# Optimization experiments

Measured on AMD Instinct MI355X. Metric: run time of the kernel, lower is better.

Reference implementation:

```python
import jax, jax.numpy as jnp
import numpy as np

KERNEL = 5
STRIDE = 1
DN = ('NHWC', 'HWIO', 'NHWC')
PRIOR_VAR = 0.01


def setup_inputs() -> dict:
    key = jax.random.key(0)
    k1, k2, k3 = jax.random.split(key, 3)
    mu_in = jax.random.normal(k1, (32, 224, 224, 3), dtype=jnp.float32)
    # GlorotNormal-ish scale for a 5x5x3 -> 64 kernel
    w_mu = jax.random.normal(k2, (5, 5, 3, 64), dtype=jnp.float32) * 0.12
    # original init: uniform in [min_sigma, ini_sigma] = [-4.6, -2.25]
    w_sigma = jax.random.uniform(k3, (64,), dtype=jnp.float32, minval=-4.6, maxval=-2.25)
    return {"mu_in": mu_in, "w_mu": w_mu, "w_sigma": w_sigma}


def reference(mu_in, w_mu, w_sigma):
    # KL regularizer: broadcast of (64,) logvar against (5,5,3,64) mu, mean over all
    kl = 0.5 * jnp.mean(
        jnp.log(PRIOR_VAR) - 1.0 - w_sigma
        + jax.nn.softplus(w_sigma) / PRIOR_VAR
        + jnp.square(w_mu) / PRIOR_VAR
    )

    w_sigma_2 = jax.nn.softplus(w_sigma)  # log(1+exp(w_sigma))

    # Mean path: standard conv2d, VALID, stride 1, NHWC
    mu_out = jax.lax.conv_general_dilated(
        mu_in, w_mu, (STRIDE, STRIDE), 'VALID', dimension_numbers=DN
    )  # [B, Ho, Wo, K]

    # Variance path: per-output-location sum over the k*k*C patch of x^2 / x_dim.
    # Same math as the original extract_patches + reduce_sum, but computed as a
    # channel-summed box filter on x^2 (no im2col materialization).
    C = mu_in.shape[-1]
    x_dim = jnp.asarray(KERNEL * KERNEL * C, mu_in.dtype)
    ones_k = jnp.ones((KERNEL, KERNEL, C, 1), mu_in.dtype)
    sq = jax.lax.conv_general_dilated(
        jnp.square(mu_in), ones_k, (STRIDE, STRIDE), 'VALID', dimension_numbers=DN
    ) / x_dim  # [B, Ho, Wo, 1]

    Sigma_out = jax.nn.softplus(w_sigma_2 * sq)  # broadcast -> [B, Ho, Wo, K]
    return (mu_out, Sigma_out, kl)
```

## Files before the change

### kernel.cpp

```cpp
#include <hip/hip_runtime.h>
#include <math.h>

#define BATCH 32
#define HIN   224
#define WIN   224
#define CIN   3
#define KOUT  64
#define RK    5
#define HOUT  220
#define WOUT  220

#define NTOT ((size_t)BATCH * HOUT * WOUT * KOUT)

typedef float  v4f    __attribute__((ext_vector_type(4)));
typedef short  short8 __attribute__((ext_vector_type(8)));

#define WS_WF_FRAGS 768
#define WS_WSG_OFF  12288

__device__ __forceinline__ float exp2_hw(float x) { float r; asm("v_exp_f32 %0, %1" : "=v"(r) : "v"(x)); return r; }
__device__ __forceinline__ float log2_hw(float x) { float r; asm("v_log_f32 %0, %1" : "=v"(r) : "v"(x)); return r; }
#define LOG2E 1.44269504088896f
#define LN2   0.69314718055995f

__device__ __forceinline__ float softplus_hw(float x) {
    float t = exp2_hw(-fabsf(x) * LOG2E);
    return fmaxf(x, 0.0f) + LN2 * log2_hw(1.0f + t);
}
__device__ __forceinline__ float softplus_pos(float y) {
    return y + LN2 * log2_hw(1.0f + exp2_hw(-y * LOG2E));
}
__device__ __forceinline__ short f2bf(float x) {
    unsigned u = __float_as_uint(x);
    u = (u + 0x7FFFu + ((u >> 16) & 1u)) >> 16;
    return (short)u;
}

__global__ __launch_bounds__(256) void vdp_prep_kernel(
    const float* __restrict__ w_mu, const float* __restrict__ w_sigma,
    void* __restrict__ ws, float* __restrict__ out)
{
    __shared__ float red[4];
    short8* wf = (short8*)ws;
    float* wsg = (float*)((char*)ws + WS_WSG_OFF);
    const int t = threadIdx.x;

    for (int f = t; f < WS_WF_FRAGS; f += 256) {
        const int s  = f >> 8;
        const int nb = (f >> 6) & 3;
        const int l  = f & 63;
        const int ch = nb * 16 + (l & 15);
        const int h2 = l >> 4;
        short8 r;
        #pragma unroll
        for (int i = 0; i < 8; ++i) {
            const int k = s * 32 + h2 * 8 + i;
            const int kh = k >> 4, inner = k & 15;
            float v = 0.0f;
            if (inner < 15 && k < 80) {
                const int kw = inner / 3;
                const int c  = inner - kw * 3;
                v = w_mu[((kh * 5 + kw) * 3 + c) * KOUT + ch];
            }
            r[i] = f2bf(v);
        }
        wf[f] = r;
    }
    if (t < KOUT) wsg[t] = softplus_hw(w_sigma[t]);

    float s = 0.0f;
    for (int i = t; i < RK * RK * CIN * KOUT; i += 256) {
        const float v = w_mu[i];
        s = fmaf(v, v, s);
    }
    float u = s * (100.0f / 4800.0f);
    if (t < KOUT) {
        const float wsv = w_sigma[t];
        u += (-wsv + softplus_hw(wsv) * 100.0f) * (1.0f / 64.0f);
    }
    #pragma unroll
    for (int off = 32; off > 0; off >>= 1)
        u += __shfl_down(u, off, 64);
    if ((t & 63) == 0) red[t >> 6] = u;
    __syncthreads();
    if (t == 0) {
        const float U = red[0] + red[1] + red[2] + red[3];
        out[2 * NTOT] = 0.5f * (-4.6051701860f - 1.0f + U);
    }
}

__global__ __launch_bounds__(256, 4) void vdp_conv_kernel(
    const float* __restrict__ mu_in, const void* __restrict__ ws, float* __restrict__ out)
{
    __shared__ float s_row[8][112];
    __shared__ float s_ssq[8][40];
    __shared__ float s_sq[4][32];

    const int tid  = threadIdx.x;
    const int lane = tid & 63;
    const int wid  = tid >> 6;
    const int p    = lane & 15;
    const int h2   = lane >> 4;

    const int b  = blockIdx.z;
    const int r0 = blockIdx.y * 4;
    const int x0 = blockIdx.x * 32;

    const short8* wfg = (const short8*)ws;
    short8 wf[12];
    #pragma unroll
    for (int f = 0; f < 12; ++f) wf[f] = wfg[f * 64 + lane];
    const float* wsg_g = (const float*)((const char*)ws + WS_WSG_OFF);
    const v4f wsg_kg = *(const v4f*)(wsg_g + p * 4);

    const size_t inbase = ((size_t)b * HIN + r0) * (WIN * CIN);
    for (int idx = tid; idx < 8 * 112; idx += 256) {
        const int r = idx / 112, c = idx - r * 112;
        int f = x0 * 3 + c; if (f > WIN * CIN - 1) f = WIN * CIN - 1;
        s_row[r][c] = mu_in[inbase + (size_t)r * (WIN * CIN) + f];
    }
    __syncthreads();

    for (int idx = tid; idx < 8 * 36; idx += 256) {
        const int r = idx / 36, px = idx - r * 36;
        const float a0 = s_row[r][3 * px], a1 = s_row[r][3 * px + 1], a2 = s_row[r][3 * px + 2];
        s_ssq[r][px] = fmaf(a0, a0, fmaf(a1, a1, a2 * a2));
    }
    __syncthreads();

    if (tid < 128) {
        const int orow = tid >> 5, pc = tid & 31;
        float a = 0.0f;
        #pragma unroll
        for (int kh = 0; kh < RK; ++kh)
            #pragma unroll
            for (int kw = 0; kw < RK; ++kw)
                a += s_ssq[orow + kh][pc + kw];
        s_sq[orow][pc] = a * (1.0f / 75.0f);
    }
    __syncthreads();

    const int rt = wid;
    const size_t rowbase = (((size_t)b * HOUT + r0 + rt) * WOUT + x0) * KOUT;

    #pragma unroll
    for (int g = 0; g < 2; ++g) {
        short8 pf[3];
        #pragma unroll
        for (int s = 0; s < 3; ++s) {
            int ridx = rt + 2 * s + (h2 >> 1);
            ridx = ridx > 7 ? 7 : ridx;
            const float* rp = &s_row[ridx][3 * (16 * g + p) + 8 * (h2 & 1)];
            short8 r;
            #pragma unroll
            for (int i = 0; i < 8; ++i) r[i] = f2bf(rp[i]);
            pf[s] = r;
        }
        v4f acc[4];
        #pragma unroll
        for (int nb = 0; nb < 4; ++nb) {
            v4f a = {0.0f, 0.0f, 0.0f, 0.0f};
            #pragma unroll
            for (int s = 0; s < 3; ++s)
                a = __builtin_amdgcn_mfma_f32_16x16x32_bf16(wf[s * 4 + nb], pf[s], a, 0, 0, 0);
            acc[nb] = a;
        }
        if (x0 + 16 * g + p < WOUT) {
            float* mp = out + rowbase + (size_t)(16 * g + p) * KOUT + h2 * 4;
            #pragma unroll
            for (int nb = 0; nb < 4; ++nb)
                *(v4f*)(mp + nb * 16) = acc[nb];
        }
    }

    float* sp = out + NTOT + rowbase + p * 4;
    #pragma unroll
    for (int q = 0; q < 8; ++q) {
        const int px = 4 * q + h2;
        if (x0 + px < WOUT) {
            const float sq = s_sq[rt][px];
            v4f sg;
            sg.x = softplus_pos(wsg_kg.x * sq);
            sg.y = softplus_pos(wsg_kg.y * sq);
            sg.z = softplus_pos(wsg_kg.z * sq);
            sg.w = softplus_pos(wsg_kg.w * sq);
            *(v4f*)(sp + (size_t)px * KOUT) = sg;
        }
    }
}

extern "C" void kernel_launch(void* const* d_in, const int* in_sizes, int n_in,
                              void* d_out, int out_size, void* d_ws, size_t ws_size,
                              hipStream_t stream)
{
    (void)in_sizes; (void)n_in; (void)ws_size; (void)out_size;
    const float* mu_in   = (const float*)d_in[0];
    const float* w_mu    = (const float*)d_in[1];
    const float* w_sigma = (const float*)d_in[2];
    float* out = (float*)d_out;

    vdp_prep_kernel<<<1, 256, 0, stream>>>(w_mu, w_sigma, d_ws, out);
    dim3 grid(7, HOUT / 4, BATCH);
    vdp_conv_kernel<<<grid, 256, 0, stream>>>(mu_in, d_ws, out);
}
```

Measured before the change: 211.4 us.

## Enlarge conv tile to 16x32 outputs and clamp edge tiles instead of masking

Each block now computes 16 output rows instead of 4. Every wave loops over 4 rows, so each block loads a 20-row input patch and less halo is reloaded. Edge tiles are shifted inward so the per-pixel bounds checks on stores disappear, at the cost of recomputing and rewriting some overlapping outputs. The grid shrinks by a factor of four, which lowers the number of blocks available for occupancy and increases the work per block.

```diff
diff --git a/kernel.cpp b/kernel.cpp
--- a/kernel.cpp
+++ b/kernel.cpp
@@ -10,6 +10,11 @@
 #define HOUT  220
 #define WOUT  220
 
+#define TH     16
+#define TW     32
+#define PATCH_H (TH + RK - 1)
+#define PATCH_W (TW + RK - 1)
+#define SROW_F  112
 #define NTOT ((size_t)BATCH * HOUT * WOUT * KOUT)
 
 typedef float  v4f    __attribute__((ext_vector_type(4)));
@@ -92,9 +97,9 @@
 __global__ __launch_bounds__(256, 4) void vdp_conv_kernel(
     const float* __restrict__ mu_in, const void* __restrict__ ws, float* __restrict__ out)
 {
-    __shared__ float s_row[8][112];
-    __shared__ float s_ssq[8][40];
-    __shared__ float s_sq[4][32];
+    __shared__ float s_row[PATCH_H][SROW_F];
+    __shared__ float s_ssq[PATCH_H][40];
+    __shared__ float s_sq[TH][TW];
 
     const int tid  = threadIdx.x;
     const int lane = tid & 63;
@@ -102,9 +107,9 @@
     const int p    = lane & 15;
     const int h2   = lane >> 4;
 
-    const int b  = blockIdx.z;
-    const int r0 = blockIdx.y * 4;
-    const int x0 = blockIdx.x * 32;
+    const int b = blockIdx.z;
+    int ho0 = blockIdx.y * TH; if (ho0 > HOUT - TH) ho0 = HOUT - TH;
+    int wo0 = blockIdx.x * TW; if (wo0 > WOUT - TW) wo0 = WOUT - TW;
 
     const short8* wfg = (const short8*)ws;
     short8 wf[12];
@@ -113,23 +118,25 @@
     const float* wsg_g = (const float*)((const char*)ws + WS_WSG_OFF);
     const v4f wsg_kg = *(const v4f*)(wsg_g + p * 4);
 
-    const size_t inbase = ((size_t)b * HIN + r0) * (WIN * CIN);
-    for (int idx = tid; idx < 8 * 112; idx += 256) {
-        const int r = idx / 112, c = idx - r * 112;
-        int f = x0 * 3 + c; if (f > WIN * CIN - 1) f = WIN * CIN - 1;
-        s_row[r][c] = mu_in[inbase + (size_t)r * (WIN * CIN) + f];
-    }
-    __syncthreads();
-
-    for (int idx = tid; idx < 8 * 36; idx += 256) {
-        const int r = idx / 36, px = idx - r * 36;
+    const size_t inbase = ((size_t)b * HIN + ho0) * (WIN * CIN) + wo0 * CIN;
+    for (int idx = tid; idx < PATCH_H * SROW_F; idx += 256) {
+        const int r = idx / SROW_F, c = idx - r * SROW_F;
+        float v = 0.0f;
+        if (c < PATCH_W * CIN) v = mu_in[inbase + (size_t)r * (WIN * CIN) + c];
+        s_row[r][c] = v;
+    }
+    __syncthreads();
+
+    for (int idx = tid; idx < PATCH_H * PATCH_W; idx += 256) {
+        const int r = idx / PATCH_W, px = idx - r * PATCH_W;
         const float a0 = s_row[r][3 * px], a1 = s_row[r][3 * px + 1], a2 = s_row[r][3 * px + 2];
         s_ssq[r][px] = fmaf(a0, a0, fmaf(a1, a1, a2 * a2));
     }
     __syncthreads();
 
-    if (tid < 128) {
-        const int orow = tid >> 5, pc = tid & 31;
+    #pragma unroll
+    for (int h = 0; h < 2; ++h) {
+        const int orow = (tid >> 5) + h * 8, pc = tid & 31;
         float a = 0.0f;
         #pragma unroll
         for (int kh = 0; kh < RK; ++kh)
@@ -140,44 +147,43 @@
     }
     __syncthreads();
 
-    const int rt = wid;
-    const size_t rowbase = (((size_t)b * HOUT + r0 + rt) * WOUT + x0) * KOUT;
-
-    #pragma unroll
-    for (int g = 0; g < 2; ++g) {
-        short8 pf[3];
-        #pragma unroll
-        for (int s = 0; s < 3; ++s) {
-            int ridx = rt + 2 * s + (h2 >> 1);
-            ridx = ridx > 7 ? 7 : ridx;
-            const float* rp = &s_row[ridx][3 * (16 * g + p) + 8 * (h2 & 1)];
-            short8 r;
-            #pragma unroll
-            for (int i = 0; i < 8; ++i) r[i] = f2bf(rp[i]);
-            pf[s] = r;
-        }
-        v4f acc[4];
-        #pragma unroll
-        for (int nb = 0; nb < 4; ++nb) {
-            v4f a = {0.0f, 0.0f, 0.0f, 0.0f};
-            #pragma unroll
-            for (int s = 0; s < 3; ++s)
-                a = __builtin_amdgcn_mfma_f32_16x16x32_bf16(wf[s * 4 + nb], pf[s], a, 0, 0, 0);
-            acc[nb] = a;
-        }
-        if (x0 + 16 * g + p < WOUT) {
+    #pragma unroll 1
+    for (int j = 0; j < 4; ++j) {
+        const int rt = (wid << 2) | j;
+        const size_t rowbase = (((size_t)b * HOUT + ho0 + rt) * WOUT + wo0) * KOUT;
+
+        #pragma unroll
+        for (int g = 0; g < 2; ++g) {
+            short8 pf[3];
+            #pragma unroll
+            for (int s = 0; s < 3; ++s) {
+                int ridx = rt + 2 * s + (h2 >> 1);
+                ridx = ridx > PATCH_H - 1 ? PATCH_H - 1 : ridx;
+                const float* rp = &s_row[ridx][3 * (16 * g + p) + 8 * (h2 & 1)];
+                short8 r;
+                #pragma unroll
+                for (int i = 0; i < 8; ++i) r[i] = f2bf(rp[i]);
+                pf[s] = r;
+            }
+            v4f acc[4];
+            #pragma unroll
+            for (int nb = 0; nb < 4; ++nb) {
+                v4f a = {0.0f, 0.0f, 0.0f, 0.0f};
+                #pragma unroll
+                for (int s = 0; s < 3; ++s)
+                    a = __builtin_amdgcn_mfma_f32_16x16x32_bf16(wf[s * 4 + nb], pf[s], a, 0, 0, 0);
+                acc[nb] = a;
+            }
             float* mp = out + rowbase + (size_t)(16 * g + p) * KOUT + h2 * 4;
             #pragma unroll
             for (int nb = 0; nb < 4; ++nb)
                 *(v4f*)(mp + nb * 16) = acc[nb];
         }
-    }
-
-    float* sp = out + NTOT + rowbase + p * 4;
-    #pragma unroll
-    for (int q = 0; q < 8; ++q) {
-        const int px = 4 * q + h2;
-        if (x0 + px < WOUT) {
+
+        float* sp = out + NTOT + rowbase + p * 4;
+        #pragma unroll
+        for (int q = 0; q < 8; ++q) {
+            const int px = (q << 2) | h2;
             const float sq = s_sq[rt][px];
             v4f sg;
             sg.x = softplus_pos(wsg_kg.x * sq);
@@ -200,6 +206,6 @@
     float* out = (float*)d_out;
 
     vdp_prep_kernel<<<1, 256, 0, stream>>>(w_mu, w_sigma, d_ws, out);
-    dim3 grid(7, HOUT / 4, BATCH);
+    dim3 grid((WOUT + TW - 1) / TW, (HOUT + TH - 1) / TH, BATCH);
     vdp_conv_kernel<<<grid, 256, 0, stream>>>(mu_in, d_ws, out);
 }
```

New measurement: 198.1 us. 1.07x faster.
